# Kernel optimization log

Hardware: AMD Instinct MI355X
Metric: run time of the kernel (lower is better)

The kernel has to match this reference:

```python
import jax, jax.numpy as jnp
import numpy as np

IH, IW = 32, 32
HEADS = 8
DIM_HEAD = 64
SCALE = DIM_HEAD ** -0.5


def _make_relative_index():
    # Matches torch buffer: ceil Euclidean distance between all pairs of 2D coords.
    ii, jj = np.meshgrid(np.arange(IH), np.arange(IW), indexing='ij')
    coords = np.stack([ii.ravel(), jj.ravel()])  # [2, n]
    rel = coords[:, :, None] - coords[:, None, :]  # [2, n, n]
    dist = np.ceil(np.sqrt(rel[0] ** 2 + rel[1] ** 2))
    return jnp.asarray(dist.astype(np.int32).ravel())  # [n*n]


def setup_inputs() -> dict:
    key = jax.random.key(0)
    k1, k2, k3, k4 = jax.random.split(key, 4)
    b, n, inp = 32, IH * IW, 512
    inner = HEADS * DIM_HEAD
    diag = int(np.ceil(np.sqrt((IH - 1) ** 2 + (IW - 1) ** 2)))
    return {
        'x': jax.random.normal(k1, (b, n, inp), jnp.float32),
        'w_qkv': jax.random.normal(k2, (inp, inner * 3), jnp.float32) * (inp ** -0.5),
        'bias_table': jax.random.normal(k3, (diag + 1, HEADS), jnp.float32) * 0.02,
        'w_out': jax.random.normal(k4, (inner, 512), jnp.float32) * (inner ** -0.5),
        'b_out': jnp.zeros((512,), jnp.float32),
        'relative_index': _make_relative_index(),
    }


def reference(x, w_qkv, bias_table, w_out, b_out, relative_index):
    b, n, _ = x.shape
    qkv = x @ w_qkv  # [b, n, 3*inner]
    q, k, v = jnp.split(qkv, 3, axis=-1)
    def to_heads(t):
        return t.reshape(b, n, HEADS, DIM_HEAD).transpose(0, 2, 1, 3)  # b h n d
    q, k, v = to_heads(q), to_heads(k), to_heads(v)
    dots = jnp.einsum('bhid,bhjd->bhij', q, k) * SCALE  # [b, h, n, n]
    # gather relative bias: [n*n, h] -> [1, h, n, n]
    rel_bias = bias_table[relative_index].reshape(n, n, HEADS).transpose(2, 0, 1)
    attn = jax.nn.softmax(dots + rel_bias[None], axis=-1)
    out = jnp.einsum('bhij,bhjd->bhid', attn, v)  # b h n d
    out = out.transpose(0, 2, 1, 3).reshape(b, n, HEADS * DIM_HEAD)
    return out @ w_out + b_out
```

## Files before the change

kernel.cpp:

```cpp
#include <hip/hip_runtime.h>
#include <hip/hip_bf16.h>
#include <cstdint>

typedef __bf16 bf16_t;
typedef bf16_t bf16x8 __attribute__((ext_vector_type(8)));
typedef float f32x4 __attribute__((ext_vector_type(4)));
typedef float f32x16 __attribute__((ext_vector_type(16)));
typedef unsigned u32x4 __attribute__((ext_vector_type(4)));

#define MFMA16(a, b, c) __builtin_amdgcn_mfma_f32_16x16x32_bf16(a, b, c, 0, 0, 0)
#define MFMA32(a, b, c) __builtin_amdgcn_mfma_f32_32x32x16_bf16(a, b, c, 0, 0, 0)

#define GLOAD_LDS16(g, l)                                                  \
    __builtin_amdgcn_global_load_lds(                                      \
        (const __attribute__((address_space(1))) unsigned*)(g),            \
        (__attribute__((address_space(3))) unsigned*)(l), 16, 0, 0)

constexpr int LDK = 72;

#define QSCALE 0.1803368801f
#define LOG2E 1.44269504f

__global__ void zero_out(unsigned short* __restrict__ out, long n) {
    long i = (long)blockIdx.x * 256 + threadIdx.x;
    if (i < n) out[i] = 0;
}

__global__ void detect_dtype(const unsigned* __restrict__ x,
                             int* __restrict__ flag) {
    if (threadIdx.x == 0 && blockIdx.x == 0) {
        int cnt = 0;
        for (int i = 0; i < 1024; ++i) {
            unsigned e = (x[i] >> 7) & 0xFF;
            cnt += (e > 100 && e < 150) ? 1 : 0;
        }
        *flag = (cnt > 512) ? 1 : 0;
    }
}

__global__ __launch_bounds__(256) void convert_x(const void* __restrict__ in,
                                                 bf16_t* __restrict__ out,
                                                 const int* __restrict__ flagp) {
    const int fl = *flagp;
    long i = ((long)blockIdx.x * 256 + threadIdx.x) * 8;
    if (fl) {
        *(bf16x8*)&out[i] = *(const bf16x8*)&((const bf16_t*)in)[i];
    } else {
        f32x4 lo = *(const f32x4*)&((const float*)in)[i];
        f32x4 hi = *(const f32x4*)&((const float*)in)[i + 4];
        bf16x8 v;
#pragma unroll
        for (int e = 0; e < 4; ++e) {
            v[e] = (bf16_t)lo[e];
            v[e + 4] = (bf16_t)hi[e];
        }
        *(bf16x8*)&out[i] = v;
    }
}

__global__ void transpose_flex(const void* __restrict__ in,
                               bf16_t* __restrict__ out, int R, int C,
                               const int* __restrict__ flagp, int scale_rows) {
    const int fl = *flagp;
    __shared__ bf16_t tile[32][33];
    int c0 = blockIdx.x * 32, r0 = blockIdx.y * 32;
    int x = threadIdx.x, y = threadIdx.y;
#pragma unroll
    for (int i = 0; i < 4; ++i) {
        long idx = (long)(r0 + y + 8 * i) * C + c0 + x;
        float fv = fl ? (float)((const bf16_t*)in)[idx]
                      : ((const float*)in)[idx];
        if (c0 + x < scale_rows) fv *= QSCALE;
        tile[y + 8 * i][x] = (bf16_t)fv;
    }
    __syncthreads();
#pragma unroll
    for (int i = 0; i < 4; ++i)
        out[(long)(c0 + y + 8 * i) * R + r0 + x] = tile[x][y + 8 * i];
}

__global__ __launch_bounds__(256) void build_bias_perm(
    const int* __restrict__ rel_index, const void* __restrict__ bias_table,
    bf16_t* __restrict__ perm, const int* __restrict__ flagp) {
    const int fl = *flagp;
    const int jt = blockIdx.x;
    const int qb = blockIdx.y;
    const int t = threadIdx.x;
    const int lane = t & 63;
    const int h = (t >> 6) + 4 * blockIdx.z;
    const int i = qb * 32 + (lane & 31);
    const int hi = lane >> 5;
    bf16_t out[16];
#pragma unroll
    for (int r = 0; r < 16; ++r) {
        int j = jt * 32 + (r & 3) + 8 * (r >> 2) + 4 * hi;
        int ridx = rel_index[i * 1024 + j];
        ridx = ridx < 0 ? 0 : (ridx > 44 ? 44 : ridx);
        float bv = fl ? (float)((const bf16_t*)bias_table)[ridx * 8 + h]
                      : ((const float*)bias_table)[ridx * 8 + h];
        out[r] = (bf16_t)(bv * LOG2E);
    }
    long off = (((long)(h * 32 + qb) * 32 + jt) << 10) + lane * 16;
    *(uint4*)&perm[off] = *(uint4*)&out[0];
    *(uint4*)&perm[off + 8] = *(uint4*)&out[8];
}

template <bool BIAS, bool OUTFLEX>
__global__ __launch_bounds__(256) void gemm_lds(
    const bf16_t* __restrict__ A, const bf16_t* __restrict__ Bt, int K,
    int lda, long a_row0, void* __restrict__ C, int ldc, long c_row0,
    const void* __restrict__ bias, const int* __restrict__ flagp) {
    const int fl = *flagp;
    __shared__ bf16_t a_lds[128 * 64];
    __shared__ bf16_t b_lds[128 * 64];
    int t = threadIdx.x;
    int wave = t >> 6, lane = t & 63;
    int m16 = lane & 15, quad = lane >> 4;
    int wr = wave >> 1, wc = wave & 1;
    long m0 = (long)blockIdx.y * 128;
    int n0 = blockIdx.x * 128;

    const int c_base = wave * 256 + lane;

    f32x4 acc[4][4] = {};

    for (int ks = 0; ks < K; ks += 64) {
#pragma unroll
        for (int i = 0; i < 4; ++i) {
            int c = c_base;
            c = wave * 256 + i * 64 + lane;
            int row = c >> 3, kc = (c & 7) << 3;
            GLOAD_LDS16(&A[(a_row0 + m0 + row) * (long)lda + ks + kc],
                        &a_lds[row * 64 + kc]);
            GLOAD_LDS16(&Bt[(long)(n0 + row) * K + ks + kc],
                        &b_lds[row * 64 + kc]);
        }
        __syncthreads();
#pragma unroll
        for (int kf = 0; kf < 2; ++kf) {
            bf16x8 af[4], bfr[4];
#pragma unroll
            for (int mb = 0; mb < 4; ++mb)
                af[mb] = *(const bf16x8*)&a_lds[(wr * 64 + mb * 16 + m16) * 64 +
                                                kf * 32 + quad * 8];
#pragma unroll
            for (int nb = 0; nb < 4; ++nb)
                bfr[nb] = *(const bf16x8*)&b_lds[(wc * 64 + nb * 16 + m16) * 64 +
                                                 kf * 32 + quad * 8];
#pragma unroll
            for (int mb = 0; mb < 4; ++mb)
#pragma unroll
                for (int nb = 0; nb < 4; ++nb)
                    acc[mb][nb] = MFMA16(af[mb], bfr[nb], acc[mb][nb]);
        }
        __syncthreads();
    }

#pragma unroll
    for (int mb = 0; mb < 4; ++mb) {
#pragma unroll
        for (int nb = 0; nb < 4; ++nb) {
            int col = n0 + wc * 64 + nb * 16 + m16;
#pragma unroll
            for (int r = 0; r < 4; ++r) {
                long row = m0 + wr * 64 + mb * 16 + quad * 4 + r;
                float v = acc[mb][nb][r];
                if (BIAS) {
                    float bb = fl ? (float)((const bf16_t*)bias)[col]
                                  : ((const float*)bias)[col];
                    v += bb;
                }
                long off = (c_row0 + row) * (long)ldc + col;
                if (OUTFLEX && !fl)
                    ((float*)C)[off] = v;
                else
                    ((bf16_t*)C)[off] = (bf16_t)v;
            }
        }
    }
}

template <bool AFLEX, bool BIAS, bool OUTFLEX>
__global__ __launch_bounds__(256) void gemm128(
    const void* __restrict__ A, const bf16_t* __restrict__ Bt, int K, int lda,
    long a_row0, void* __restrict__ C, int ldc, long c_row0,
    const void* __restrict__ bias, const int* __restrict__ flagp) {
    const int fl = *flagp;
    __shared__ bf16_t a_lds[128 * LDK];
    __shared__ bf16_t b_lds[128 * LDK];
    int t = threadIdx.x;
    int wave = t >> 6, lane = t & 63;
    int m16 = lane & 15, quad = lane >> 4;
    int wr = wave >> 1, wc = wave & 1;
    long m0 = (long)blockIdx.y * 128;
    int n0 = blockIdx.x * 128;

    f32x4 acc[4][4] = {};

    for (int ks = 0; ks < K; ks += 64) {
#pragma unroll
        for (int i = 0; i < 4; ++i) {
            int c = t + 256 * i;
            int row = c >> 3;
            int kc = (c & 7) << 3;
            bf16x8 av;
            if (AFLEX && !fl) {
                const float* Af = (const float*)A;
                long base = (a_row0 + m0 + row) * (long)lda + ks + kc;
                f32x4 lo = *(const f32x4*)&Af[base];
                f32x4 hi = *(const f32x4*)&Af[base + 4];
#pragma unroll
                for (int e = 0; e < 4; ++e) {
                    av[e] = (bf16_t)lo[e];
                    av[e + 4] = (bf16_t)hi[e];
                }
            } else {
                av = *(const bf16x8*)&(
                    (const bf16_t*)A)[(a_row0 + m0 + row) * (long)lda + ks + kc];
            }
            *(bf16x8*)&a_lds[row * LDK + kc] = av;
            *(bf16x8*)&b_lds[row * LDK + kc] =
                *(const bf16x8*)&Bt[(long)(n0 + row) * K + ks + kc];
        }
        __syncthreads();
#pragma unroll
        for (int kf = 0; kf < 2; ++kf) {
            bf16x8 af[4], bfr[4];
#pragma unroll
            for (int mb = 0; mb < 4; ++mb)
                af[mb] = *(const bf16x8*)&a_lds[(wr * 64 + mb * 16 + m16) * LDK +
                                                kf * 32 + quad * 8];
#pragma unroll
            for (int nb = 0; nb < 4; ++nb)
                bfr[nb] = *(const bf16x8*)&b_lds[(wc * 64 + nb * 16 + m16) * LDK +
                                                 kf * 32 + quad * 8];
#pragma unroll
            for (int mb = 0; mb < 4; ++mb)
#pragma unroll
                for (int nb = 0; nb < 4; ++nb)
                    acc[mb][nb] = MFMA16(af[mb], bfr[nb], acc[mb][nb]);
        }
        __syncthreads();
    }

#pragma unroll
    for (int mb = 0; mb < 4; ++mb) {
#pragma unroll
        for (int nb = 0; nb < 4; ++nb) {
            int col = n0 + wc * 64 + nb * 16 + m16;
#pragma unroll
            for (int r = 0; r < 4; ++r) {
                long row = m0 + wr * 64 + mb * 16 + quad * 4 + r;
                float v = acc[mb][nb][r];
                if (BIAS) {
                    float bb = fl ? (float)((const bf16_t*)bias)[col]
                                  : ((const float*)bias)[col];
                    v += bb;
                }
                long off = (c_row0 + row) * (long)ldc + col;
                if (OUTFLEX && !fl)
                    ((float*)C)[off] = v;
                else
                    ((bf16_t*)C)[off] = (bf16_t)v;
            }
        }
    }
}

__global__ __launch_bounds__(256) void flash_attn2(
    bf16_t* __restrict__ qkv, const bf16_t* __restrict__ bias_perm) {
    __shared__ bf16_t k_lds[2][64 * 64];
    __shared__ bf16_t v_lds[2][64 * 64];

    const int t = threadIdx.x;
    const int lane = t & 63, wave = t >> 6;
    const int l31 = lane & 31, hi = lane >> 5;
    const int h = blockIdx.y, b = blockIdx.z;
    bf16_t* base = qkv + (long)b * 1024 * 1536;
    bf16_t* qb = base + h * 64;
    const bf16_t* kb = base + 512 + h * 64;
    const bf16_t* vb = base + 1024 + h * 64;
    const int qblk = blockIdx.x * 4 + wave;
    const int q0w = qblk * 32;
    const bf16_t* bp = bias_perm + (((long)(h * 32 + qblk)) << 15) + lane * 16;

    bf16x8 qf[4];
#pragma unroll
    for (int s = 0; s < 4; ++s)
        qf[s] = *(const bf16x8*)&qb[(long)(q0w + l31) * 1536 + s * 16 + hi * 8];

    f32x16 oacc0 = {}, oacc1 = {};
    float mrun = -1e30f, lrun = 0.f;

    const int sr0 = t >> 3, sg0 = t & 7;
    const int sr1 = sr0 + 32;

    {
        bf16x8 k0 = *(const bf16x8*)&kb[(long)sr0 * 1536 + sg0 * 8];
        bf16x8 k1 = *(const bf16x8*)&kb[(long)sr1 * 1536 + sg0 * 8];
        bf16x8 v0 = *(const bf16x8*)&vb[(long)sr0 * 1536 + sg0 * 8];
        bf16x8 v1 = *(const bf16x8*)&vb[(long)sr1 * 1536 + sg0 * 8];
        *(bf16x8*)&k_lds[0][sr0 * 64 + ((sg0 ^ (sr0 & 7)) << 3)] = k0;
        *(bf16x8*)&k_lds[0][sr1 * 64 + ((sg0 ^ (sr1 & 7)) << 3)] = k1;
#pragma unroll
        for (int e = 0; e < 8; ++e) {
            int d0 = sg0 * 8 + e;
            v_lds[0][d0 * 64 + (((sr0 >> 3) ^ (d0 & 7)) << 3) + (sr0 & 7)] = v0[e];
            v_lds[0][d0 * 64 + (((sr1 >> 3) ^ (d0 & 7)) << 3) + (sr1 & 7)] = v1[e];
        }
    }
    __syncthreads();

    for (int tt = 0; tt < 16; ++tt) {
        const int cur = tt & 1;
        bf16x8 kn0 = {}, kn1 = {}, vn0 = {}, vn1 = {};
        if (tt < 15) {
            long j0n = (long)(tt + 1) * 64;
            kn0 = *(const bf16x8*)&kb[(j0n + sr0) * 1536 + sg0 * 8];
            kn1 = *(const bf16x8*)&kb[(j0n + sr1) * 1536 + sg0 * 8];
            vn0 = *(const bf16x8*)&vb[(j0n + sr0) * 1536 + sg0 * 8];
            vn1 = *(const bf16x8*)&vb[(j0n + sr1) * 1536 + sg0 * 8];
        }
        const bf16_t* bt = bp + ((long)tt << 11);
        uint4 bv[4];
        bv[0] = *(const uint4*)(bt);
        bv[1] = *(const uint4*)(bt + 8);
        bv[2] = *(const uint4*)(bt + 1024);
        bv[3] = *(const uint4*)(bt + 1024 + 8);

#pragma unroll
        for (int js = 0; js < 2; ++js) {
            f32x16 s = {};
            const int krow = js * 32 + l31;
#pragma unroll
            for (int st = 0; st < 4; ++st) {
                bf16x8 kf = *(const bf16x8*)&k_lds[cur][krow * 64 +
                             (((st * 2 + hi) ^ (krow & 7)) << 3)];
                s = MFMA32(kf, qf[st], s);
            }
            bf16_t bb[16];
            *(uint4*)&bb[0] = bv[2 * js];
            *(uint4*)&bb[8] = bv[2 * js + 1];
            float sv[16];
#pragma unroll
            for (int r = 0; r < 16; ++r) sv[r] = s[r] + (float)bb[r];
            float mx = sv[0];
#pragma unroll
            for (int r = 1; r < 16; ++r) mx = fmaxf(mx, sv[r]);
            {
                float o0 = mx, o1 = mx;
                asm("" : "+v"(o1));
                asm("v_permlane32_swap_b32 %0, %1" : "+v"(o0), "+v"(o1));
                mx = fmaxf(o0, o1);
            }
            if (!__all(mx <= mrun + 11.0f)) {
                float mnew = fmaxf(mrun, mx);
                float al = __builtin_amdgcn_exp2f(mrun - mnew);
                mrun = mnew;
                lrun *= al;
#pragma unroll
                for (int r = 0; r < 16; ++r) {
                    oacc0[r] *= al;
                    oacc1[r] *= al;
                }
            }
            float s0 = 0.f, s1 = 0.f, s2 = 0.f, s3 = 0.f;
#pragma unroll
            for (int r = 0; r < 16; ++r) {
                sv[r] = __builtin_amdgcn_exp2f(sv[r] - mrun);
                if ((r & 3) == 0) s0 += sv[r];
                else if ((r & 3) == 1) s1 += sv[r];
                else if ((r & 3) == 2) s2 += sv[r];
                else s3 += sv[r];
            }
            float rs = (s0 + s1) + (s2 + s3);
            {
                float o0 = rs, o1 = rs;
                asm("" : "+v"(o1));
                asm("v_permlane32_swap_b32 %0, %1" : "+v"(o0), "+v"(o1));
                rs = o0 + o1;
            }
            lrun += rs;
            unsigned dw[8];
#pragma unroll
            for (int g = 0; g < 4; ++g) {
                unsigned da, db;
                asm("v_cvt_pk_bf16_f32 %0, %1, %2"
                    : "=v"(da) : "v"(sv[4 * g]), "v"(sv[4 * g + 1]));
                asm("v_cvt_pk_bf16_f32 %0, %1, %2"
                    : "=v"(db) : "v"(sv[4 * g + 2]), "v"(sv[4 * g + 3]));
                dw[2 * g] = da;
                dw[2 * g + 1] = db;
            }
#pragma unroll
            for (int kk = 0; kk < 2; ++kk) {
                asm("v_permlane32_swap_b32 %0, %1"
                    : "+v"(dw[4 * kk + 0]), "+v"(dw[4 * kk + 2]));
                asm("v_permlane32_swap_b32 %0, %1"
                    : "+v"(dw[4 * kk + 1]), "+v"(dw[4 * kk + 3]));
            }
#pragma unroll
            for (int kk = 0; kk < 2; ++kk) {
                u32x4 uv;
                uv[0] = dw[4 * kk + 0];
                uv[1] = dw[4 * kk + 1];
                uv[2] = dw[4 * kk + 2];
                uv[3] = dw[4 * kk + 3];
                bf16x8 pa = __builtin_bit_cast(bf16x8, uv);
#pragma unroll
                for (int db2 = 0; db2 < 2; ++db2) {
                    const int vrow = db2 * 32 + l31;
                    bf16x8 vf = *(const bf16x8*)&v_lds[cur][vrow * 64 +
                                 (((js * 4 + kk * 2 + hi) ^ (vrow & 7)) << 3)];
                    if (db2 == 0)
                        oacc0 = MFMA32(pa, vf, oacc0);
                    else
                        oacc1 = MFMA32(pa, vf, oacc1);
                }
            }
        }
        if (tt < 15) {
            const int nb = cur ^ 1;
            *(bf16x8*)&k_lds[nb][sr0 * 64 + ((sg0 ^ (sr0 & 7)) << 3)] = kn0;
            *(bf16x8*)&k_lds[nb][sr1 * 64 + ((sg0 ^ (sr1 & 7)) << 3)] = kn1;
#pragma unroll
            for (int e = 0; e < 8; ++e) {
                int d0 = sg0 * 8 + e;
                v_lds[nb][d0 * 64 + (((sr0 >> 3) ^ (d0 & 7)) << 3) + (sr0 & 7)] =
                    vn0[e];
                v_lds[nb][d0 * 64 + (((sr1 >> 3) ^ (d0 & 7)) << 3) + (sr1 & 7)] =
                    vn1[e];
            }
        }
        __syncthreads();
    }

    float linv = 1.0f / lrun;
#pragma unroll
    for (int r = 0; r < 16; ++r) {
        int row = (r & 3) + 8 * (r >> 2) + 4 * hi;
        float lr = __int_as_float(
            __builtin_amdgcn_ds_bpermute(row << 2, __float_as_int(linv)));
        qb[(long)(q0w + row) * 1536 + l31] = (bf16_t)(oacc0[r] * lr);
        qb[(long)(q0w + row) * 1536 + 32 + l31] = (bf16_t)(oacc1[r] * lr);
    }
}

extern "C" void kernel_launch(void* const* d_in, const int* in_sizes, int n_in,
                              void* d_out, int out_size, void* d_ws,
                              size_t ws_size, hipStream_t stream) {
    const void* x = nullptr;
    const void* w_qkv = nullptr;
    const void* bias_table = nullptr;
    const void* w_out = nullptr;
    const void* b_out = nullptr;
    const void* rel_raw = nullptr;
    for (int i = 0; i < n_in; ++i) {
        switch (in_sizes[i]) {
            case 16777216: x = d_in[i]; break;
            case 786432:  w_qkv = d_in[i]; break;
            case 360:     bias_table = d_in[i]; break;
            case 262144:  w_out = d_in[i]; break;
            case 512:     b_out = d_in[i]; break;
            case 1048576: rel_raw = d_in[i]; break;
            default: break;
        }
    }
    if (!x || !w_qkv || !bias_table || !w_out || !b_out || !rel_raw) {
        x = d_in[0]; w_qkv = d_in[1]; bias_table = d_in[2];
        w_out = d_in[3]; b_out = d_in[4]; rel_raw = d_in[5];
    }
    const int* rel_index = (const int*)rel_raw;

    char* ws = (char*)d_ws;
    bf16_t* wqkvT = (bf16_t*)ws;
    bf16_t* woutT = (bf16_t*)(ws + 1572864);
    int* flag = (int*)(ws + 1572864 + 524288);
    bf16_t* rel_bias = (bf16_t*)(ws + 1572864 + 524288 + 256);
    const size_t fixed = 1572864 + 524288 + 256 + 16777216;
    const size_t xbf_bytes = (size_t)32 * 1024 * 512 * sizeof(bf16_t);
    const size_t per_batch = (size_t)1024 * 1536 * sizeof(bf16_t);

    if (ws_size < fixed + per_batch) {
        long n = (long)out_size;
        long nblk = (n + 255) / 256;
        if (nblk > 0)
            zero_out<<<(unsigned)nblk, 256, 0, stream>>>(
                (unsigned short*)d_out, n);
        return;
    }

    bool have_xbf = ws_size >= fixed + xbf_bytes + per_batch;
    bf16_t* x_bf = (bf16_t*)(ws + fixed);
    bf16_t* qkv = have_xbf ? (bf16_t*)(ws + fixed + xbf_bytes)
                           : (bf16_t*)(ws + fixed);

    size_t avail = ws_size - fixed - (have_xbf ? xbf_bytes : 0);
    int chunk = (int)(avail / per_batch);
    if (chunk > 32) chunk = 32;
    if (chunk < 1) chunk = 1;
    while (32 % chunk) --chunk;

    detect_dtype<<<1, 64, 0, stream>>>((const unsigned*)x, flag);
    transpose_flex<<<dim3(1536 / 32, 512 / 32), dim3(32, 8), 0, stream>>>(
        w_qkv, wqkvT, 512, 1536, flag, 512);
    transpose_flex<<<dim3(512 / 32, 512 / 32), dim3(32, 8), 0, stream>>>(
        w_out, woutT, 512, 512, flag, 0);
    build_bias_perm<<<dim3(32, 32, 2), 256, 0, stream>>>(
        rel_index, bias_table, rel_bias, flag);
    if (have_xbf)
        convert_x<<<8192, 256, 0, stream>>>(x, x_bf, flag);

    for (int b0 = 0; b0 < 32; b0 += chunk) {
        long row0 = (long)b0 * 1024;
        int mrows = chunk * 1024;
        if (have_xbf) {
            gemm_lds<false, false>
                <<<dim3(1536 / 128, mrows / 128), 256, 0, stream>>>(
                    x_bf, wqkvT, 512, 512, row0, qkv, 1536, 0, nullptr, flag);
        } else {
            gemm128<true, false, false>
                <<<dim3(1536 / 128, mrows / 128), 256, 0, stream>>>(
                    x, wqkvT, 512, 512, row0, qkv, 1536, 0, nullptr, flag);
        }
        flash_attn2<<<dim3(8, 8, chunk), 256, 0, stream>>>(qkv, rel_bias);
        gemm_lds<true, true>
            <<<dim3(512 / 128, mrows / 128), 256, 0, stream>>>(
                qkv, woutT, 512, 1536, 0, d_out, 512, row0, b_out, flag);
    }
}
```

Baseline: 474.2 us.

## Pre-transpose V per head and use transposed-V flash attention kernel

Adds a transpose_v kernel that writes V for each batch/head into a contiguous [d, n] layout using a swizzled LDS tile. A new flash_attn3 kernel loads that transposed V with async global-to-LDS copies and feeds it straight to the PV MFMA, and it skips the online-softmax rescale unless the running max grows by more than a threshold. This is meant to remove the in-kernel V transposition or strided V access cost in attention. The price is an extra kernel launch, an extra pass over V in memory, and more workspace, which can shrink the batch chunk size. The old path is kept as a fallback when workspace is short.

Measured after the change: 462.4 us. -2.5%, faster.

```diff
diff --git a/kernel.cpp b/kernel.cpp
--- a/kernel.cpp
+++ b/kernel.cpp
@@ -103,6 +103,38 @@
     long off = (((long)(h * 32 + qb) * 32 + jt) << 10) + lane * 16;
     *(uint4*)&perm[off] = *(uint4*)&out[0];
     *(uint4*)&perm[off + 8] = *(uint4*)&out[8];
+}
+
+__global__ __launch_bounds__(256) void transpose_v(
+    const bf16_t* __restrict__ qkv, bf16_t* __restrict__ vt) {
+    __shared__ bf16_t tile[64 * 64];
+    const int jt = blockIdx.x;
+    const int bh = blockIdx.y;
+    const int b = bh >> 3, h = bh & 7;
+    const bf16_t* src = qkv + (long)b * 1024 * 1536 + 1024 + h * 64;
+    const int t = threadIdx.x;
+    const int r = t >> 3, c8 = t & 7;
+    const int j0 = jt * 64;
+#pragma unroll
+    for (int rep = 0; rep < 2; ++rep) {
+        int jj = r + 32 * rep;
+        *(bf16x8*)&tile[jj * 64 + ((c8 ^ (jj >> 3)) << 3)] =
+            *(const bf16x8*)&src[(long)(j0 + jj) * 1536 + c8 * 8];
+    }
+    __syncthreads();
+#pragma unroll
+    for (int rep = 0; rep < 2; ++rep) {
+        int dd = r + 32 * rep;
+        int jc = c8 * 8;
+        bf16_t o[8];
+#pragma unroll
+        for (int e = 0; e < 8; ++e) {
+            int row = jc + e;
+            o[e] = tile[row * 64 + (((dd >> 3) ^ (row >> 3)) << 3) + (dd & 7)];
+        }
+        *(bf16x8*)&vt[((long)bh << 16) + (long)dd * 1024 + j0 + jc] =
+            *(bf16x8*)&o[0];
+    }
 }
 
 template <bool BIAS, bool OUTFLEX>
@@ -120,15 +152,12 @@
     long m0 = (long)blockIdx.y * 128;
     int n0 = blockIdx.x * 128;
 
-    const int c_base = wave * 256 + lane;
-
     f32x4 acc[4][4] = {};
 
     for (int ks = 0; ks < K; ks += 64) {
 #pragma unroll
         for (int i = 0; i < 4; ++i) {
-            int c = c_base;
-            c = wave * 256 + i * 64 + lane;
+            int c = wave * 256 + i * 64 + lane;
             int row = c >> 3, kc = (c & 7) << 3;
             GLOAD_LDS16(&A[(a_row0 + m0 + row) * (long)lda + ks + kc],
                         &a_lds[row * 64 + kc]);
@@ -264,6 +293,173 @@
                     ((bf16_t*)C)[off] = (bf16_t)v;
             }
         }
+    }
+}
+
+__global__ __launch_bounds__(256) void flash_attn3(
+    bf16_t* __restrict__ qkv, const bf16_t* __restrict__ vt,
+    const bf16_t* __restrict__ bias_perm) {
+    __shared__ bf16_t k_lds[2][64 * 64];
+    __shared__ bf16_t v_lds[2][64 * 64];
+
+    const int t = threadIdx.x;
+    const int lane = t & 63, wave = t >> 6;
+    const int l31 = lane & 31, hi = lane >> 5;
+    const int h = blockIdx.y, b = blockIdx.z;
+    bf16_t* base = qkv + (long)b * 1024 * 1536;
+    bf16_t* qb = base + h * 64;
+    const bf16_t* kb = base + 512 + h * 64;
+    const bf16_t* vtb = vt + ((long)(b * 8 + h) << 16);
+    const int qblk = blockIdx.x * 4 + wave;
+    const int q0w = qblk * 32;
+    const bf16_t* bp = bias_perm + (((long)(h * 32 + qblk)) << 15) + lane * 16;
+
+    bf16x8 qf[4];
+#pragma unroll
+    for (int s = 0; s < 4; ++s)
+        qf[s] = *(const bf16x8*)&qb[(long)(q0w + l31) * 1536 + s * 16 + hi * 8];
+
+    f32x16 oacc0 = {}, oacc1 = {};
+    float mrun = -1e30f, lrun = 0.f;
+
+    const int srow = t >> 3, pc = t & 7;
+    const int kc0 = (pc ^ (srow & 7)) << 3;
+
+    {
+        GLOAD_LDS16(&kb[(long)srow * 1536 + kc0],
+                    &k_lds[0][srow * 64 + pc * 8]);
+        GLOAD_LDS16(&kb[(long)(srow + 32) * 1536 + kc0],
+                    &k_lds[0][(srow + 32) * 64 + pc * 8]);
+        GLOAD_LDS16(&vtb[(long)srow * 1024 + kc0],
+                    &v_lds[0][srow * 64 + pc * 8]);
+        GLOAD_LDS16(&vtb[(long)(srow + 32) * 1024 + kc0],
+                    &v_lds[0][(srow + 32) * 64 + pc * 8]);
+    }
+    __syncthreads();
+
+    for (int tt = 0; tt < 16; ++tt) {
+        const int cur = tt & 1;
+        const bf16_t* bt = bp + ((long)tt << 11);
+        uint4 bv[4];
+        bv[0] = *(const uint4*)(bt);
+        bv[1] = *(const uint4*)(bt + 8);
+        bv[2] = *(const uint4*)(bt + 1024);
+        bv[3] = *(const uint4*)(bt + 1024 + 8);
+        if (tt < 15) {
+            const int nb = cur ^ 1;
+            long j0n = (long)(tt + 1) * 64;
+            GLOAD_LDS16(&kb[(j0n + srow) * 1536 + kc0],
+                        &k_lds[nb][srow * 64 + pc * 8]);
+            GLOAD_LDS16(&kb[(j0n + srow + 32) * 1536 + kc0],
+                        &k_lds[nb][(srow + 32) * 64 + pc * 8]);
+            GLOAD_LDS16(&vtb[(long)srow * 1024 + j0n + kc0],
+                        &v_lds[nb][srow * 64 + pc * 8]);
+            GLOAD_LDS16(&vtb[(long)(srow + 32) * 1024 + j0n + kc0],
+                        &v_lds[nb][(srow + 32) * 64 + pc * 8]);
+        }
+
+#pragma unroll
+        for (int js = 0; js < 2; ++js) {
+            f32x16 s = {};
+            const int krow = js * 32 + l31;
+#pragma unroll
+            for (int st = 0; st < 4; ++st) {
+                bf16x8 kf = *(const bf16x8*)&k_lds[cur][krow * 64 +
+                             (((st * 2 + hi) ^ (krow & 7)) << 3)];
+                s = MFMA32(kf, qf[st], s);
+            }
+            bf16_t bb[16];
+            *(uint4*)&bb[0] = bv[2 * js];
+            *(uint4*)&bb[8] = bv[2 * js + 1];
+            float sv[16];
+#pragma unroll
+            for (int r = 0; r < 16; ++r) sv[r] = s[r] + (float)bb[r];
+            float mx = sv[0];
+#pragma unroll
+            for (int r = 1; r < 16; ++r) mx = fmaxf(mx, sv[r]);
+            {
+                float o0 = mx, o1 = mx;
+                asm("" : "+v"(o1));
+                asm("v_permlane32_swap_b32 %0, %1" : "+v"(o0), "+v"(o1));
+                mx = fmaxf(o0, o1);
+            }
+            if (!__all(mx <= mrun + 11.0f)) {
+                float mnew = fmaxf(mrun, mx);
+                float al = __builtin_amdgcn_exp2f(mrun - mnew);
+                mrun = mnew;
+                lrun *= al;
+#pragma unroll
+                for (int r = 0; r < 16; ++r) {
+                    oacc0[r] *= al;
+                    oacc1[r] *= al;
+                }
+            }
+            float s0 = 0.f, s1 = 0.f, s2 = 0.f, s3 = 0.f;
+#pragma unroll
+            for (int r = 0; r < 16; ++r) {
+                sv[r] = __builtin_amdgcn_exp2f(sv[r] - mrun);
+                if ((r & 3) == 0) s0 += sv[r];
+                else if ((r & 3) == 1) s1 += sv[r];
+                else if ((r & 3) == 2) s2 += sv[r];
+                else s3 += sv[r];
+            }
+            float rs = (s0 + s1) + (s2 + s3);
+            {
+                float o0 = rs, o1 = rs;
+                asm("" : "+v"(o1));
+                asm("v_permlane32_swap_b32 %0, %1" : "+v"(o0), "+v"(o1));
+                rs = o0 + o1;
+            }
+            lrun += rs;
+            unsigned dw[8];
+#pragma unroll
+            for (int g = 0; g < 4; ++g) {
+                unsigned da, db;
+                asm("v_cvt_pk_bf16_f32 %0, %1, %2"
+                    : "=v"(da) : "v"(sv[4 * g]), "v"(sv[4 * g + 1]));
+                asm("v_cvt_pk_bf16_f32 %0, %1, %2"
+                    : "=v"(db) : "v"(sv[4 * g + 2]), "v"(sv[4 * g + 3]));
+                dw[2 * g] = da;
+                dw[2 * g + 1] = db;
+            }
+#pragma unroll
+            for (int kk = 0; kk < 2; ++kk) {
+                asm("v_permlane32_swap_b32 %0, %1"
+                    : "+v"(dw[4 * kk + 0]), "+v"(dw[4 * kk + 2]));
+                asm("v_permlane32_swap_b32 %0, %1"
+                    : "+v"(dw[4 * kk + 1]), "+v"(dw[4 * kk + 3]));
+            }
+#pragma unroll
+            for (int kk = 0; kk < 2; ++kk) {
+                u32x4 uv;
+                uv[0] = dw[4 * kk + 0];
+                uv[1] = dw[4 * kk + 1];
+                uv[2] = dw[4 * kk + 2];
+                uv[3] = dw[4 * kk + 3];
+                bf16x8 pa = __builtin_bit_cast(bf16x8, uv);
+#pragma unroll
+                for (int db2 = 0; db2 < 2; ++db2) {
+                    const int vrow = db2 * 32 + l31;
+                    bf16x8 vf = *(const bf16x8*)&v_lds[cur][vrow * 64 +
+                                 (((js * 4 + kk * 2 + hi) ^ (vrow & 7)) << 3)];
+                    if (db2 == 0)
+                        oacc0 = MFMA32(pa, vf, oacc0);
+                    else
+                        oacc1 = MFMA32(pa, vf, oacc1);
+                }
+            }
+        }
+        __syncthreads();
+    }
+
+    float linv = 1.0f / lrun;
+#pragma unroll
+    for (int r = 0; r < 16; ++r) {
+        int row = (r & 3) + 8 * (r >> 2) + 4 * hi;
+        float lr = __int_as_float(
+            __builtin_amdgcn_ds_bpermute(row << 2, __float_as_int(linv)));
+        qb[(long)(q0w + row) * 1536 + l31] = (bf16_t)(oacc0[r] * lr);
+        qb[(long)(q0w + row) * 1536 + 32 + l31] = (bf16_t)(oacc1[r] * lr);
     }
 }
 
@@ -479,9 +675,10 @@
     bf16_t* rel_bias = (bf16_t*)(ws + 1572864 + 524288 + 256);
     const size_t fixed = 1572864 + 524288 + 256 + 16777216;
     const size_t xbf_bytes = (size_t)32 * 1024 * 512 * sizeof(bf16_t);
-    const size_t per_batch = (size_t)1024 * 1536 * sizeof(bf16_t);
-
-    if (ws_size < fixed + per_batch) {
+    const size_t qkv_pb = (size_t)1024 * 1536 * sizeof(bf16_t);
+    const size_t vt_pb = (size_t)8 * 64 * 1024 * sizeof(bf16_t);
+
+    if (ws_size < fixed + qkv_pb) {
         long n = (long)out_size;
         long nblk = (n + 255) / 256;
         if (nblk > 0)
@@ -490,16 +687,19 @@
         return;
     }
 
-    bool have_xbf = ws_size >= fixed + xbf_bytes + per_batch;
+    bool have_xbf = ws_size >= fixed + xbf_bytes + qkv_pb;
+    bool have_vt = ws_size >= fixed + xbf_bytes + qkv_pb + vt_pb;
     bf16_t* x_bf = (bf16_t*)(ws + fixed);
     bf16_t* qkv = have_xbf ? (bf16_t*)(ws + fixed + xbf_bytes)
                            : (bf16_t*)(ws + fixed);
 
     size_t avail = ws_size - fixed - (have_xbf ? xbf_bytes : 0);
-    int chunk = (int)(avail / per_batch);
+    size_t pb = have_vt ? (qkv_pb + vt_pb) : qkv_pb;
+    int chunk = (int)(avail / pb);
     if (chunk > 32) chunk = 32;
     if (chunk < 1) chunk = 1;
     while (32 % chunk) --chunk;
+    bf16_t* vt = (bf16_t*)((char*)qkv + (size_t)chunk * qkv_pb);
 
     detect_dtype<<<1, 64, 0, stream>>>((const unsigned*)x, flag);
     transpose_flex<<<dim3(1536 / 32, 512 / 32), dim3(32, 8), 0, stream>>>(
@@ -523,7 +723,13 @@
                 <<<dim3(1536 / 128, mrows / 128), 256, 0, stream>>>(
                     x, wqkvT, 512, 512, row0, qkv, 1536, 0, nullptr, flag);
         }
-        flash_attn2<<<dim3(8, 8, chunk), 256, 0, stream>>>(qkv, rel_bias);
+        if (have_vt) {
+            transpose_v<<<dim3(16, chunk * 8), 256, 0, stream>>>(qkv, vt);
+            flash_attn3<<<dim3(8, 8, chunk), 256, 0, stream>>>(qkv, vt,
+                                                               rel_bias);
+        } else {
+            flash_attn2<<<dim3(8, 8, chunk), 256, 0, stream>>>(qkv, rel_bias);
+        }
         gemm_lds<true, true>
             <<<dim3(512 / 128, mrows / 128), 256, 0, stream>>>(
                 qkv, woutT, 512, 1536, 0, d_out, 512, row0, b_out, flag);
```
